# Optimization experiments

Hardware: AMD Instinct MI355X
Metric: run time of the kernel (lower is better)

The kernel has to match this reference:

```python
import jax, jax.numpy as jnp
import numpy as np

N = 100000   # n_nodes
E = 800000   # n_edges
IN = 128
HID = 128
OUT = 40
EPS = 1e-5   # BatchNorm1d eps


def setup_inputs() -> dict:
    key = jax.random.key(0)
    ks = jax.random.split(key, 16)
    def w(k, i, o):
        return jax.random.normal(k, (i, o), jnp.float32) / np.sqrt(i).astype(np.float32)
    return {
        "x": jax.random.normal(ks[0], (N, IN), jnp.float32),
        "edge_index": jax.random.randint(ks[1], (2, E), 0, N, dtype=jnp.int64),
        # SAGEConv weights: Wl acts on aggregated neighbors, Wr on root features
        "Wl0": w(ks[2], IN, HID),  "Wr0": w(ks[3], IN, HID),
        "Wl1": w(ks[4], HID, HID), "Wr1": w(ks[5], HID, HID),
        "Wl2": w(ks[6], HID, OUT), "Wr2": w(ks[7], HID, OUT),
        "b2": jnp.zeros((OUT,), jnp.float32),  # bias only on last layer
        # BatchNorm params for layers 0,1 (last layer has no BN)
        "g0": jnp.ones((HID,), jnp.float32), "be0": jnp.zeros((HID,), jnp.float32),
        "g1": jnp.ones((HID,), jnp.float32), "be1": jnp.zeros((HID,), jnp.float32),
    }


def _sage_conv(x, src, dst, Wl, Wr, b=None):
    # mean aggregation of source messages at destination nodes
    msg = x[src]                                             # [E, d] gather
    agg = jax.ops.segment_sum(msg, dst, num_segments=N)      # [N, d]
    cnt = jax.ops.segment_sum(jnp.ones((src.shape[0],), x.dtype), dst,
                              num_segments=N)                # [N]
    mean = agg / jnp.maximum(cnt, 1.0)[:, None]
    out = mean @ Wl + x @ Wr
    if b is not None:
        out = out + b
    return out


def _batch_norm(h, gamma, beta):
    # training-mode BN over node dim, biased variance (matches torch BatchNorm1d)
    mu = h.mean(axis=0)
    var = h.var(axis=0)
    return (h - mu) * jax.lax.rsqrt(var + EPS) * gamma + beta


def reference(x, edge_index, Wl0, Wr0, Wl1, Wr1, Wl2, Wr2, b2, g0, be0, g1, be1):
    src, dst = edge_index[0], edge_index[1]
    h = _sage_conv(x, src, dst, Wl0, Wr0)
    h = jax.nn.relu(_batch_norm(h, g0, be0))
    h = _sage_conv(h, src, dst, Wl1, Wr1)
    h = jax.nn.relu(_batch_norm(h, g1, be1))
    h = _sage_conv(h, src, dst, Wl2, Wr2, b2)
    return h
```

## Files before the change

### kernel.cpp

```cpp
#include <hip/hip_runtime.h>
#include <hip/hip_bf16.h>

#define N_NODES 100000
#define N_EDGES 800000
#define EPS 1e-5f
#define NBANK 32
#define HB_BLOCKS 256
#define HB_PER 3125
#define NBUCK 250
#define BUCKET_N 400
#define MROW 68

typedef __attribute__((ext_vector_type(8))) short short8;
typedef __attribute__((ext_vector_type(4))) float floatx4;

__device__ __forceinline__ unsigned short f2b(float f) {
    unsigned int u = __float_as_uint(f);
    u = (u + 0x7fffu + ((u >> 16) & 1u)) >> 16;
    return (unsigned short)u;
}
__device__ __forceinline__ float blo(unsigned int u) { return __uint_as_float(u << 16); }
__device__ __forceinline__ float bhi(unsigned int u) { return __uint_as_float(u & 0xffff0000u); }
__device__ __forceinline__ float b2f(unsigned short s) {
    return __uint_as_float(((unsigned int)s) << 16);
}

__device__ __forceinline__ void pack_one(const float* __restrict__ Wl,
                                         const float* __restrict__ Wr,
                                         unsigned short* __restrict__ out,
                                         int Hreal, int NCT, int tid) {
    int i = tid & 7;
    int lane = (tid >> 3) & 63;
    int q = tid >> 9;
    int c = q % NCT;
    int t = q / NCT;
    int k = t * 32 + (lane >> 4) * 8 + i;
    int n = c * 16 + (lane & 15);
    float v = 0.f;
    if (n < Hreal) v = (k < 128) ? Wl[k * Hreal + n] : Wr[(k - 128) * Hreal + n];
    out[tid] = f2b(v);
}

__global__ void __launch_bounds__(256) prep_k(const float* __restrict__ x,
                                              unsigned short* __restrict__ o,
                                              const int* __restrict__ dst,
                                              unsigned int* __restrict__ bhist,
                                              const float* __restrict__ Wl0, const float* __restrict__ Wr0,
                                              const float* __restrict__ Wl1, const float* __restrict__ Wr1,
                                              const float* __restrict__ Wl2, const float* __restrict__ Wr2,
                                              unsigned short* __restrict__ W0p,
                                              unsigned short* __restrict__ W1p,
                                              unsigned short* __restrict__ W2p) {
    int b = blockIdx.x;
    if (b < 12500) {
        int i = b * 256 + threadIdx.x;
        float4 v = ((const float4*)x)[i];
        ushort4 r;
        r.x = f2b(v.x); r.y = f2b(v.y); r.z = f2b(v.z); r.w = f2b(v.w);
        ((ushort4*)o)[i] = r;
        return;
    }
    if (b < 12756) {
        __shared__ unsigned int lh[NBUCK];
        int hb = b - 12500;
        if (threadIdx.x < NBUCK) lh[threadIdx.x] = 0;
        __syncthreads();
        int start = hb * HB_PER;
        for (int i = threadIdx.x; i < HB_PER; i += 256) {
            int d = dst[start + i];
            atomicAdd(&lh[(unsigned int)d / BUCKET_N], 1u);
        }
        __syncthreads();
        if (threadIdx.x < NBUCK) bhist[threadIdx.x * HB_BLOCKS + hb] = lh[threadIdx.x];
        return;
    }
    int tid = (b - 12756) * 256 + threadIdx.x;
    if (tid < 32768) pack_one(Wl0, Wr0, W0p, 128, 8, tid);
    else if (tid < 65536) pack_one(Wl1, Wr1, W1p, 128, 8, tid - 32768);
    else pack_one(Wl2, Wr2, W2p, 40, 3, tid - 65536);
}

__global__ void __launch_bounds__(1024) bscan(unsigned int* __restrict__ A) {
    __shared__ unsigned int part[1024];
    int t = threadIdx.x;
    unsigned int v[64];
    unsigned int s = 0;
    if (t < 1000) {
#pragma unroll
        for (int i = 0; i < 64; i++) { v[i] = A[t * 64 + i]; s += v[i]; }
    }
    part[t] = s;
    __syncthreads();
    for (int off = 1; off < 1024; off <<= 1) {
        unsigned int add = (t >= off) ? part[t - off] : 0u;
        __syncthreads();
        part[t] += add;
        __syncthreads();
    }
    if (t < 1000) {
        unsigned int base = part[t] - s;
#pragma unroll
        for (int i = 0; i < 64; i++) { unsigned int old = v[i]; A[t * 64 + i] = base; base += old; }
    }
}

__global__ void __launch_bounds__(256) bscatter(const int* __restrict__ src,
                                                const int* __restrict__ dst,
                                                const unsigned int* __restrict__ boffs,
                                                unsigned int* __restrict__ ebuf) {
    __shared__ unsigned int cur[NBUCK];
    if (threadIdx.x < NBUCK) cur[threadIdx.x] = boffs[threadIdx.x * HB_BLOCKS + blockIdx.x];
    __syncthreads();
    int start = blockIdx.x * HB_PER;
    for (int i = threadIdx.x; i < HB_PER; i += 256) {
        int d = dst[start + i];
        int s = src[start + i];
        unsigned int b = (unsigned int)d / BUCKET_N;
        unsigned int dl = (unsigned int)d - b * BUCKET_N;
        unsigned int pos = atomicAdd(&cur[b], 1u);
        ebuf[pos] = (unsigned int)s | (dl << 17);
    }
}

__global__ void __launch_bounds__(256) bucket_sort_k(const unsigned int* __restrict__ ebuf,
                                                     const unsigned int* __restrict__ bhist,
                                                     unsigned int* __restrict__ rowptr,
                                                     int* __restrict__ srclist) {
    __shared__ unsigned int cntl[BUCKET_N];
    __shared__ unsigned int psum[256];
    int g = blockIdx.x;
    int t = threadIdx.x;
    unsigned int estart = bhist[g * HB_BLOCKS];
    unsigned int eend = (g == NBUCK - 1) ? N_EDGES : bhist[(g + 1) * HB_BLOCKS];

    if (t < BUCKET_N) cntl[t] = 0u;
    if (t + 256 < BUCKET_N) cntl[t + 256] = 0u;
    __syncthreads();

    for (unsigned int i = estart + t; i < eend; i += 256)
        atomicAdd(&cntl[ebuf[i] >> 17], 1u);
    __syncthreads();

    unsigned int l0 = 0, l1 = 0, s = 0;
    int base = t * 2;
    if (base < BUCKET_N) {
        unsigned int v0 = cntl[base];
        unsigned int v1 = (base + 1 < BUCKET_N) ? cntl[base + 1] : 0u;
        l0 = 0; l1 = v0; s = v0 + v1;
    }
    psum[t] = s;
    __syncthreads();
    for (int off = 1; off < 256; off <<= 1) {
        unsigned int add = (t >= off) ? psum[t - off] : 0u;
        __syncthreads();
        psum[t] += add;
        __syncthreads();
    }
    unsigned int tb = psum[t] - s;
    if (base < BUCKET_N) {
        unsigned int o0 = tb + l0;
        unsigned int o1 = tb + l1;
        cntl[base] = o0;
        rowptr[g * BUCKET_N + base] = estart + o0;
        if (base + 1 < BUCKET_N) {
            cntl[base + 1] = o1;
            rowptr[g * BUCKET_N + base + 1] = estart + o1;
        }
    }
    if (g == NBUCK - 1 && t == 0) rowptr[N_NODES] = N_EDGES;
    __syncthreads();

    for (unsigned int i = estart + t; i < eend; i += 256) {
        unsigned int p = ebuf[i];
        unsigned int pos = atomicAdd(&cntl[p >> 17], 1u);
        srclist[estart + pos] = (int)(p & 0x1FFFFu);
    }
}

template<int BN>
__device__ __forceinline__ void agg_phase16(const unsigned short* __restrict__ hb,
                                            const unsigned int* __restrict__ rowptr,
                                            const int* __restrict__ srclist,
                                            unsigned int* __restrict__ smean,
                                            const float* __restrict__ sc,
                                            const float* __restrict__ sh,
                                            int wave, int g, int l, int blockrow) {
    const uint4* hp = (const uint4*)hb;
    int nl = wave * 4 + g;
    int node = blockrow + nl;
    float f0 = 0.f, f1 = 0.f, f2 = 0.f, f3 = 0.f, f4 = 0.f, f5 = 0.f, f6 = 0.f, f7 = 0.f;
    float sc0r = 0.f, sc1r = 0.f, sc2r = 0.f, sc3r = 0.f, sc4r = 0.f, sc5r = 0.f, sc6r = 0.f, sc7r = 0.f;
    float sh0r = 0.f, sh1r = 0.f, sh2r = 0.f, sh3r = 0.f, sh4r = 0.f, sh5r = 0.f, sh6r = 0.f, sh7r = 0.f;
    if (BN) {
        const float* s0 = sc + l * 8;
        const float* s1 = sh + l * 8;
        sc0r = s0[0]; sc1r = s0[1]; sc2r = s0[2]; sc3r = s0[3];
        sc4r = s0[4]; sc5r = s0[5]; sc6r = s0[6]; sc7r = s0[7];
        sh0r = s1[0]; sh1r = s1[1]; sh2r = s1[2]; sh3r = s1[3];
        sh4r = s1[4]; sh5r = s1[5]; sh6r = s1[6]; sh7r = s1[7];
    }
    unsigned int b = rowptr[node], e = rowptr[node + 1];
    unsigned int p = b;
#define ACC8(U) { \
    if (BN) { \
        f0 += fmaxf(0.f, fmaf(blo(U.x), sc0r, sh0r)); \
        f1 += fmaxf(0.f, fmaf(bhi(U.x), sc1r, sh1r)); \
        f2 += fmaxf(0.f, fmaf(blo(U.y), sc2r, sh2r)); \
        f3 += fmaxf(0.f, fmaf(bhi(U.y), sc3r, sh3r)); \
        f4 += fmaxf(0.f, fmaf(blo(U.z), sc4r, sh4r)); \
        f5 += fmaxf(0.f, fmaf(bhi(U.z), sc5r, sh5r)); \
        f6 += fmaxf(0.f, fmaf(blo(U.w), sc6r, sh6r)); \
        f7 += fmaxf(0.f, fmaf(bhi(U.w), sc7r, sh7r)); \
    } else { \
        f0 += blo(U.x); f1 += bhi(U.x); f2 += blo(U.y); f3 += bhi(U.y); \
        f4 += blo(U.z); f5 += bhi(U.z); f6 += blo(U.w); f7 += bhi(U.w); \
    } }
    int s0 = 0, s1 = 0, s2 = 0, s3 = 0;
    bool have = (p + 4 <= e);
    if (have) { s0 = srclist[p]; s1 = srclist[p + 1]; s2 = srclist[p + 2]; s3 = srclist[p + 3]; }
    while (have) {
        uint4 u0 = hp[(size_t)s0 * 16 + l];
        uint4 u1 = hp[(size_t)s1 * 16 + l];
        uint4 u2 = hp[(size_t)s2 * 16 + l];
        uint4 u3 = hp[(size_t)s3 * 16 + l];
        p += 4;
        have = (p + 4 <= e);
        if (have) { s0 = srclist[p]; s1 = srclist[p + 1]; s2 = srclist[p + 2]; s3 = srclist[p + 3]; }
        ACC8(u0); ACC8(u1); ACC8(u2); ACC8(u3);
    }
    if (p + 2 <= e) {
        int t0 = srclist[p];
        int t1 = srclist[p + 1];
        uint4 u0 = hp[(size_t)t0 * 16 + l];
        uint4 u1 = hp[(size_t)t1 * 16 + l];
        ACC8(u0); ACC8(u1);
        p += 2;
    }
    if (p < e) {
        int t0 = srclist[p];
        uint4 u0 = hp[(size_t)t0 * 16 + l];
        ACC8(u0);
    }
#undef ACC8
    unsigned int deg = e - b;
    float r = 1.0f / (float)(deg > 1u ? deg : 1u);
    uint4 o;
    o.x = (unsigned int)f2b(f0 * r) | ((unsigned int)f2b(f1 * r) << 16);
    o.y = (unsigned int)f2b(f2 * r) | ((unsigned int)f2b(f3 * r) << 16);
    o.z = (unsigned int)f2b(f4 * r) | ((unsigned int)f2b(f5 * r) << 16);
    o.w = (unsigned int)f2b(f6 * r) | ((unsigned int)f2b(f7 * r) << 16);
    *(uint4*)&smean[nl * MROW + l * 4] = o;
}

__device__ __forceinline__ short8 bn_pack8(short8 raw, const float* __restrict__ scb,
                                           const float* __restrict__ shb, int koff) {
    short8 r;
#pragma unroll
    for (int i = 0; i < 8; i++) {
        float v = b2f((unsigned short)raw[i]);
        v = fmaxf(0.f, fmaf(v, scb[koff + i], shb[koff + i]));
        r[i] = (short)f2b(v);
    }
    return r;
}

template<int BN>
__global__ void __launch_bounds__(256) gemm2f_k(const unsigned short* __restrict__ hb,
                                                const unsigned int* __restrict__ rowptr,
                                                const int* __restrict__ srclist,
                                                const float* __restrict__ sc,
                                                const float* __restrict__ sh,
                                                const unsigned short* __restrict__ Bp,
                                                unsigned short* __restrict__ outb,
                                                float* __restrict__ sums) {
    __shared__ unsigned int smean[16 * MROW];
    __shared__ float lds_s[128];
    __shared__ float lds_s2[128];
    __shared__ float scb[128];
    __shared__ float shb[128];
    int wave = threadIdx.x >> 6;
    int lane = threadIdx.x & 63;
    int quad = lane >> 4;
    int l15 = lane & 15;
    int blockrow = blockIdx.x * 16;

    if (threadIdx.x < 128) {
        lds_s[threadIdx.x] = 0.f; lds_s2[threadIdx.x] = 0.f;
        if (BN) { scb[threadIdx.x] = sc[threadIdx.x]; shb[threadIdx.x] = sh[threadIdx.x]; }
    }
    if (BN) __syncthreads();

    agg_phase16<BN>(hb, rowptr, srclist, smean, sc, sh, wave, quad, l15, blockrow);
    __syncthreads();

    floatx4 acc[2];
    acc[0] = (floatx4){0.f, 0.f, 0.f, 0.f};
    acc[1] = (floatx4){0.f, 0.f, 0.f, 0.f};

    int r0 = blockrow + l15;

#pragma unroll
    for (int t = 0; t < 8; t++) {
        short8 a0;
        if (t < 4) {
            a0 = *(const short8*)&smean[l15 * MROW + t * 16 + quad * 4];
        } else {
            int koff = (t & 3) * 32 + quad * 8;
            short8 raw = *(const short8*)(hb + (size_t)r0 * 128 + koff);
            a0 = BN ? bn_pack8(raw, scb, shb, koff) : raw;
        }
#pragma unroll
        for (int c = 0; c < 2; c++) {
            int cidx = wave * 2 + c;
            short8 bf = *(const short8*)(Bp + ((size_t)(t * 8 + cidx) * 64 + lane) * 8);
            acc[c] = __builtin_amdgcn_mfma_f32_16x16x32_bf16(a0, bf, acc[c], 0, 0, 0);
        }
    }

#pragma unroll
    for (int c = 0; c < 2; c++) {
        int col = wave * 32 + c * 16 + l15;
        float s = 0.f, s2 = 0.f;
#pragma unroll
        for (int r = 0; r < 4; r++) {
            int row = blockrow + quad * 4 + r;
            float v = acc[c][r];
            outb[(size_t)row * 128 + col] = f2b(v);
            s += v; s2 += v * v;
        }
        s += __shfl_xor(s, 16);  s += __shfl_xor(s, 32);
        s2 += __shfl_xor(s2, 16); s2 += __shfl_xor(s2, 32);
        if (quad == 0) {
            atomicAdd(&lds_s[col], s);
            atomicAdd(&lds_s2[col], s2);
        }
    }

    __syncthreads();
    if (threadIdx.x < 128) {
        int bank = blockIdx.x & (NBANK - 1);
        atomicAdd(&sums[bank * 256 + threadIdx.x], lds_s[threadIdx.x]);
        atomicAdd(&sums[bank * 256 + 128 + threadIdx.x], lds_s2[threadIdx.x]);
    }
}

__global__ void __launch_bounds__(192) dense_k(const unsigned short* __restrict__ hb,
                                               const float* __restrict__ sc,
                                               const float* __restrict__ sh,
                                               const unsigned short* __restrict__ Bp,
                                               const float* __restrict__ bias,
                                               unsigned short* __restrict__ P,
                                               float* __restrict__ Q) {
    __shared__ float scb[128];
    __shared__ float shb[128];
    int wave = threadIdx.x >> 6;
    int lane = threadIdx.x & 63;
    int quad = lane >> 4;
    int l15 = lane & 15;
    int blockrow = blockIdx.x * 16;

    if (threadIdx.x < 128) { scb[threadIdx.x] = sc[threadIdx.x]; shb[threadIdx.x] = sh[threadIdx.x]; }
    __syncthreads();

    int r0 = blockrow + l15;
    short8 af[4];
#pragma unroll
    for (int t = 0; t < 4; t++) {
        int koff = t * 32 + quad * 8;
        short8 raw = *(const short8*)(hb + (size_t)r0 * 128 + koff);
        af[t] = bn_pack8(raw, scb, shb, koff);
    }

    floatx4 aP = (floatx4){0.f, 0.f, 0.f, 0.f};
    floatx4 aQ = (floatx4){0.f, 0.f, 0.f, 0.f};
#pragma unroll
    for (int t = 0; t < 4; t++) {
        short8 bl = *(const short8*)(Bp + ((size_t)(t * 3 + wave) * 64 + lane) * 8);
        aP = __builtin_amdgcn_mfma_f32_16x16x32_bf16(af[t], bl, aP, 0, 0, 0);
    }
#pragma unroll
    for (int t = 0; t < 4; t++) {
        short8 br = *(const short8*)(Bp + ((size_t)((t + 4) * 3 + wave) * 64 + lane) * 8);
        aQ = __builtin_amdgcn_mfma_f32_16x16x32_bf16(af[t], br, aQ, 0, 0, 0);
    }
    int col = wave * 16 + l15;
    if (col < 40) {
#pragma unroll
        for (int r = 0; r < 4; r++) {
            int row = blockrow + quad * 4 + r;
            P[(size_t)row * 40 + col] = f2b(aP[r]);
            Q[(size_t)row * 40 + col] = aQ[r] + bias[col];
        }
    }
}

__global__ void __launch_bounds__(256) agg40_k(const unsigned short* __restrict__ P,
                                               const unsigned int* __restrict__ rowptr,
                                               const int* __restrict__ srclist,
                                               const float* __restrict__ Q,
                                               float* __restrict__ out) {
    int tid = threadIdx.x;
    int g = tid >> 3;
    int l = tid & 7;
    int ll = l < 5 ? l : 0;
    int node = blockIdx.x * 32 + g;
    const uint4* pp = (const uint4*)P;
    float f0 = 0.f, f1 = 0.f, f2 = 0.f, f3 = 0.f, f4 = 0.f, f5 = 0.f, f6 = 0.f, f7 = 0.f;
    unsigned int b = rowptr[node], e = rowptr[node + 1];
    unsigned int p = b;
#define ACC8(U) { f0 += blo(U.x); f1 += bhi(U.x); f2 += blo(U.y); f3 += bhi(U.y); \
                  f4 += blo(U.z); f5 += bhi(U.z); f6 += blo(U.w); f7 += bhi(U.w); }
    int s0 = 0, s1 = 0, s2 = 0, s3 = 0;
    bool have = (p + 4 <= e);
    if (have) { s0 = srclist[p]; s1 = srclist[p + 1]; s2 = srclist[p + 2]; s3 = srclist[p + 3]; }
    while (have) {
        uint4 u0 = pp[(size_t)s0 * 5 + ll];
        uint4 u1 = pp[(size_t)s1 * 5 + ll];
        uint4 u2 = pp[(size_t)s2 * 5 + ll];
        uint4 u3 = pp[(size_t)s3 * 5 + ll];
        p += 4;
        have = (p + 4 <= e);
        if (have) { s0 = srclist[p]; s1 = srclist[p + 1]; s2 = srclist[p + 2]; s3 = srclist[p + 3]; }
        ACC8(u0); ACC8(u1); ACC8(u2); ACC8(u3);
    }
    if (p + 2 <= e) {
        int t0 = srclist[p];
        int t1 = srclist[p + 1];
        uint4 u0 = pp[(size_t)t0 * 5 + ll];
        uint4 u1 = pp[(size_t)t1 * 5 + ll];
        ACC8(u0); ACC8(u1);
        p += 2;
    }
    if (p < e) {
        int t0 = srclist[p];
        uint4 u0 = pp[(size_t)t0 * 5 + ll];
        ACC8(u0);
    }
#undef ACC8
    unsigned int deg = e - b;
    float r = 1.0f / (float)(deg > 1u ? deg : 1u);
    if (l < 5) {
        size_t base = (size_t)node * 40 + l * 8;
        float4 o1, o2;
        o1.x = f0 * r + Q[base + 0]; o1.y = f1 * r + Q[base + 1];
        o1.z = f2 * r + Q[base + 2]; o1.w = f3 * r + Q[base + 3];
        o2.x = f4 * r + Q[base + 4]; o2.y = f5 * r + Q[base + 5];
        o2.z = f6 * r + Q[base + 6]; o2.w = f7 * r + Q[base + 7];
        *(float4*)(out + base) = o1;
        *(float4*)(out + base + 4) = o2;
    }
}

__global__ void bn_finalize(const float* __restrict__ sums, const float* __restrict__ g,
                            const float* __restrict__ be, float* __restrict__ sc,
                            float* __restrict__ sh) {
    __shared__ float lds[256];
    int t = threadIdx.x;
    float s = 0.f;
#pragma unroll 8
    for (int bk = 0; bk < NBANK; bk++) s += sums[bk * 256 + t];
    lds[t] = s;
    __syncthreads();
    if (t < 128) {
        float inv_n = 1.0f / (float)N_NODES;
        float mu = lds[t] * inv_n;
        float var = lds[128 + t] * inv_n - mu * mu;
        float sf = g[t] * rsqrtf(var + EPS);
        sc[t] = sf;
        sh[t] = be[t] - mu * sf;
    }
}

extern "C" void kernel_launch(void* const* d_in, const int* in_sizes, int n_in,
                              void* d_out, int out_size, void* d_ws, size_t ws_size,
                              hipStream_t stream) {
    const float* x   = (const float*)d_in[0];
    const int* ei    = (const int*)d_in[1];
    const float* Wl0 = (const float*)d_in[2];
    const float* Wr0 = (const float*)d_in[3];
    const float* Wl1 = (const float*)d_in[4];
    const float* Wr1 = (const float*)d_in[5];
    const float* Wl2 = (const float*)d_in[6];
    const float* Wr2 = (const float*)d_in[7];
    const float* b2  = (const float*)d_in[8];
    const float* g0  = (const float*)d_in[9];
    const float* be0 = (const float*)d_in[10];
    const float* g1  = (const float*)d_in[11];
    const float* be1 = (const float*)d_in[12];

    char* ws = (char*)d_ws;
    size_t off = 0;
    auto alloc = [&](size_t bytes) -> void* {
        void* p = ws + off;
        off += (bytes + 4095) & ~(size_t)4095;
        return p;
    };

    const size_t NB16 = (size_t)N_NODES * 128 * 2;
    unsigned short* xb   = (unsigned short*)alloc(NB16);
    unsigned short* C0b  = (unsigned short*)alloc(NB16);
    unsigned short* C1b  = (unsigned short*)alloc(NB16);
    float* sums0         = (float*)alloc(NBANK * 256 * 4);
    float* sums1         = (float*)alloc(NBANK * 256 * 4);
    unsigned int* rowptr = (unsigned int*)alloc((size_t)(N_NODES + 1) * 4);
    int* srclist         = (int*)alloc((size_t)N_EDGES * 4);
    unsigned int* ebuf   = (unsigned int*)alloc((size_t)N_EDGES * 4);
    unsigned int* bhist  = (unsigned int*)alloc((size_t)NBUCK * HB_BLOCKS * 4);
    float* sc            = (float*)alloc(128 * 4);
    float* sh            = (float*)alloc(128 * 4);
    unsigned short* W0p  = (unsigned short*)alloc(8 * 8 * 64 * 8 * 2);
    unsigned short* W1p  = (unsigned short*)alloc(8 * 8 * 64 * 8 * 2);
    unsigned short* W2p  = (unsigned short*)alloc(3 * 8 * 64 * 8 * 2);

    unsigned short* P40  = C0b;
    float* Q             = (float*)xb;

    const int* srcp = ei;
    const int* dstp = ei + N_EDGES;

    hipMemsetAsync(sums0, 0, (size_t)2 * NBANK * 256 * 4, stream);

    prep_k<<<13060, 256, 0, stream>>>(x, xb, dstp, bhist,
                                      Wl0, Wr0, Wl1, Wr1, Wl2, Wr2, W0p, W1p, W2p);

    bscan<<<1, 1024, 0, stream>>>(bhist);
    bscatter<<<HB_BLOCKS, 256, 0, stream>>>(srcp, dstp, bhist, ebuf);
    bucket_sort_k<<<NBUCK, 256, 0, stream>>>(ebuf, bhist, rowptr, srclist);

    gemm2f_k<0><<<6250, 256, 0, stream>>>(xb, rowptr, srclist, nullptr, nullptr, W0p, C0b, sums0);
    bn_finalize<<<1, 256, 0, stream>>>(sums0, g0, be0, sc, sh);

    gemm2f_k<1><<<6250, 256, 0, stream>>>(C0b, rowptr, srclist, sc, sh, W1p, C1b, sums1);
    bn_finalize<<<1, 256, 0, stream>>>(sums1, g1, be1, sc, sh);

    dense_k<<<6250, 192, 0, stream>>>(C1b, sc, sh, W2p, b2, P40, Q);
    agg40_k<<<3125, 256, 0, stream>>>(P40, rowptr, srclist, Q, (float*)d_out);

    (void)in_sizes; (void)n_in; (void)out_size; (void)ws_size;
}
```

Measured before the change: 307.3 us.

## Sort nodes by degree within windows to balance aggregation wavefronts

Adds a kernel that counting-sorts nodes by in-degree (capped at 63) inside windows of 4000 nodes and produces a permutation. The two fused aggregate+GEMM kernels then process nodes in permuted order, so the 16 nodes a block handles have similar degrees and lanes in a wave finish their neighbor loops together. The cost is an extra small launch, an indirect row index for the root-feature loads and output stores (less coalesced), and a barrier that now always runs.

Result: no change. 312.3 us (+1.6%).

```diff
diff --git a/kernel.cpp b/kernel.cpp
--- a/kernel.cpp
+++ b/kernel.cpp
@@ -10,6 +10,7 @@
 #define NBUCK 250
 #define BUCKET_N 400
 #define MROW 68
+#define WIN 4000
 
 typedef __attribute__((ext_vector_type(8))) short short8;
 typedef __attribute__((ext_vector_type(4))) float floatx4;
@@ -177,6 +178,34 @@
     }
 }
 
+__global__ void __launch_bounds__(256) wsort_k(const unsigned int* __restrict__ rowptr,
+                                               int* __restrict__ perm) {
+    __shared__ unsigned int hist[64];
+    __shared__ unsigned int curs[64];
+    int base = blockIdx.x * WIN;
+    int t = threadIdx.x;
+    if (t < 64) hist[t] = 0;
+    __syncthreads();
+    for (int i = t; i < WIN; i += 256) {
+        unsigned int d = rowptr[base + i + 1] - rowptr[base + i];
+        if (d > 63u) d = 63u;
+        atomicAdd(&hist[d], 1u);
+    }
+    __syncthreads();
+    if (t == 0) {
+        unsigned int s = 0;
+#pragma unroll
+        for (int i = 0; i < 64; i++) { curs[i] = s; s += hist[i]; }
+    }
+    __syncthreads();
+    for (int i = t; i < WIN; i += 256) {
+        unsigned int d = rowptr[base + i + 1] - rowptr[base + i];
+        if (d > 63u) d = 63u;
+        unsigned int pos = atomicAdd(&curs[d], 1u);
+        perm[base + pos] = base + i;
+    }
+}
+
 template<int BN>
 __device__ __forceinline__ void agg_phase16(const unsigned short* __restrict__ hb,
                                             const unsigned int* __restrict__ rowptr,
@@ -184,10 +213,11 @@
                                             unsigned int* __restrict__ smean,
                                             const float* __restrict__ sc,
                                             const float* __restrict__ sh,
-                                            int wave, int g, int l, int blockrow) {
+                                            const int* __restrict__ pblk,
+                                            int wave, int g, int l) {
     const uint4* hp = (const uint4*)hb;
     int nl = wave * 4 + g;
-    int node = blockrow + nl;
+    int node = pblk[nl];
     float f0 = 0.f, f1 = 0.f, f2 = 0.f, f3 = 0.f, f4 = 0.f, f5 = 0.f, f6 = 0.f, f7 = 0.f;
     float sc0r = 0.f, sc1r = 0.f, sc2r = 0.f, sc3r = 0.f, sc4r = 0.f, sc5r = 0.f, sc6r = 0.f, sc7r = 0.f;
     float sh0r = 0.f, sh1r = 0.f, sh2r = 0.f, sh3r = 0.f, sh4r = 0.f, sh5r = 0.f, sh6r = 0.f, sh7r = 0.f;
@@ -268,6 +298,7 @@
 __global__ void __launch_bounds__(256) gemm2f_k(const unsigned short* __restrict__ hb,
                                                 const unsigned int* __restrict__ rowptr,
                                                 const int* __restrict__ srclist,
+                                                const int* __restrict__ perm,
                                                 const float* __restrict__ sc,
                                                 const float* __restrict__ sh,
                                                 const unsigned short* __restrict__ Bp,
@@ -278,26 +309,27 @@
     __shared__ float lds_s2[128];
     __shared__ float scb[128];
     __shared__ float shb[128];
+    __shared__ int pblk[16];
     int wave = threadIdx.x >> 6;
     int lane = threadIdx.x & 63;
     int quad = lane >> 4;
     int l15 = lane & 15;
-    int blockrow = blockIdx.x * 16;
 
     if (threadIdx.x < 128) {
         lds_s[threadIdx.x] = 0.f; lds_s2[threadIdx.x] = 0.f;
         if (BN) { scb[threadIdx.x] = sc[threadIdx.x]; shb[threadIdx.x] = sh[threadIdx.x]; }
     }
-    if (BN) __syncthreads();
-
-    agg_phase16<BN>(hb, rowptr, srclist, smean, sc, sh, wave, quad, l15, blockrow);
+    if (threadIdx.x < 16) pblk[threadIdx.x] = perm[blockIdx.x * 16 + threadIdx.x];
+    __syncthreads();
+
+    agg_phase16<BN>(hb, rowptr, srclist, smean, sc, sh, pblk, wave, quad, l15);
     __syncthreads();
 
     floatx4 acc[2];
     acc[0] = (floatx4){0.f, 0.f, 0.f, 0.f};
     acc[1] = (floatx4){0.f, 0.f, 0.f, 0.f};
 
-    int r0 = blockrow + l15;
+    int r0 = pblk[l15];
 
 #pragma unroll
     for (int t = 0; t < 8; t++) {
@@ -323,7 +355,7 @@
         float s = 0.f, s2 = 0.f;
 #pragma unroll
         for (int r = 0; r < 4; r++) {
-            int row = blockrow + quad * 4 + r;
+            int row = pblk[quad * 4 + r];
             float v = acc[c][r];
             outb[(size_t)row * 128 + col] = f2b(v);
             s += v; s2 += v * v;
@@ -506,6 +538,7 @@
     int* srclist         = (int*)alloc((size_t)N_EDGES * 4);
     unsigned int* ebuf   = (unsigned int*)alloc((size_t)N_EDGES * 4);
     unsigned int* bhist  = (unsigned int*)alloc((size_t)NBUCK * HB_BLOCKS * 4);
+    int* perm            = (int*)alloc((size_t)N_NODES * 4);
     float* sc            = (float*)alloc(128 * 4);
     float* sh            = (float*)alloc(128 * 4);
     unsigned short* W0p  = (unsigned short*)alloc(8 * 8 * 64 * 8 * 2);
@@ -527,10 +560,12 @@
     bscatter<<<HB_BLOCKS, 256, 0, stream>>>(srcp, dstp, bhist, ebuf);
     bucket_sort_k<<<NBUCK, 256, 0, stream>>>(ebuf, bhist, rowptr, srclist);
 
-    gemm2f_k<0><<<6250, 256, 0, stream>>>(xb, rowptr, srclist, nullptr, nullptr, W0p, C0b, sums0);
+    wsort_k<<<N_NODES / WIN, 256, 0, stream>>>(rowptr, perm);
+
+    gemm2f_k<0><<<6250, 256, 0, stream>>>(xb, rowptr, srclist, perm, nullptr, nullptr, W0p, C0b, sums0);
     bn_finalize<<<1, 256, 0, stream>>>(sums0, g0, be0, sc, sh);
 
-    gemm2f_k<1><<<6250, 256, 0, stream>>>(C0b, rowptr, srclist, sc, sh, W1p, C1b, sums1);
+    gemm2f_k<1><<<6250, 256, 0, stream>>>(C0b, rowptr, srclist, perm, sc, sh, W1p, C1b, sums1);
     bn_finalize<<<1, 256, 0, stream>>>(sums1, g1, be1, sc, sh);
 
     dense_k<<<6250, 192, 0, stream>>>(C1b, sc, sh, W2p, b2, P40, Q);
```
